# Optimization experiments

Measured on AMD Instinct MI355X. Metric: run time of the kernel, lower is better.

The kernel has to match this reference:

```python
import jax, jax.numpy as jnp
import numpy as np

FEA, DK, H = 768, 64, 12
B, L = 4, 1024
MASK_VAL = -2**15 + 1  # matches torch masked_fill constant


def setup_inputs() -> dict:
    key = jax.random.key(0)
    ks = jax.random.split(key, 16)
    d = {
        'qx': jax.random.normal(ks[0], (B, L, FEA), jnp.float32),
        'kx': jax.random.normal(ks[1], (B, L, FEA), jnp.float32),
        'vx': jax.random.normal(ks[2], (B, L, FEA), jnp.float32),
        'preScores': jax.random.normal(ks[3], (B, H, L, L), jnp.float32),
        'maskPAD': jax.random.randint(ks[4], (B, L, L), 0, 2, jnp.int32),
    }
    s = 1.0 / np.sqrt(FEA)
    d['WQ_w'] = jax.random.normal(ks[5], (H * DK, FEA), jnp.float32) * s
    d['WQ_b'] = jnp.zeros((H * DK,), jnp.float32)
    d['WK_w'] = jax.random.normal(ks[6], (H * DK, FEA), jnp.float32) * s
    d['WK_b'] = jnp.zeros((H * DK,), jnp.float32)
    d['WV_w'] = jax.random.normal(ks[7], (H * DK, FEA), jnp.float32) * s
    d['WV_b'] = jnp.zeros((H * DK,), jnp.float32)
    d['WO_w'] = jax.random.normal(ks[8], (FEA, H * DK), jnp.float32) * s
    d['WO_b'] = jnp.zeros((FEA,), jnp.float32)
    return d


def reference(qx, kx, vx, preScores, maskPAD,
              WQ_w, WQ_b, WK_w, WK_b, WV_w, WV_b, WO_w, WO_b):
    b, l, c = qx.shape
    # projections -> (B, H, L, dk)
    q = (qx @ WQ_w.T + WQ_b).reshape(b, l, H, DK).transpose(0, 2, 1, 3)
    k = (kx @ WK_w.T + WK_b).reshape(b, l, H, DK).transpose(0, 2, 1, 3)
    v = (vx @ WV_w.T + WV_b).reshape(b, l, H, DK).transpose(0, 2, 1, 3)
    scores = jnp.einsum('bhqd,bhkd->bhqk', q, k) / np.sqrt(DK)
    scores = scores + preScores  # RealFormer residual scores
    scores = jnp.where((maskPAD == 0)[:, None, :, :], jnp.float32(MASK_VAL), scores)
    alpha = jax.nn.softmax(scores, axis=3)  # dropout p=0 (eval/deterministic)
    z = jnp.einsum('bhqk,bhkd->bhqd', alpha, v)
    z = z.transpose(0, 2, 1, 3).reshape(b, l, H * DK)
    z = z @ WO_w.T + WO_b
    return z, scores
```

## Files before the change

kernel.cpp:

```cpp
#include <hip/hip_runtime.h>
#include <hip/hip_bf16.h>

#define B_ 4
#define L_ 1024
#define H_ 12
#define DK_ 64
#define FEA_ 768
#define MASKV (-32767.0f)

typedef __attribute__((ext_vector_type(8))) short bf16x8;
typedef __attribute__((ext_vector_type(4))) short s16x4;
typedef __attribute__((ext_vector_type(4))) float f32x4;
typedef unsigned int u32;

__device__ inline short f2bf(float x) {
  __hip_bfloat16 h = __float2bfloat16(x);
  return __builtin_bit_cast(short, h);
}

#define SZX  (4 * 1024 * 768)
#define SZW  (768 * 768)

__global__ __launch_bounds__(256) void k_cvt(
    const float* __restrict__ qx, const float* __restrict__ kx,
    const float* __restrict__ vx,
    const float* __restrict__ Wq, const float* __restrict__ Wk,
    const float* __restrict__ Wv,
    unsigned short* __restrict__ dst)
{
  const size_t SZX4 = SZX / 4, SZW4 = SZW / 4;
  const size_t total4 = 3 * SZX4 + 3 * SZW4;
  for (size_t i4 = (size_t)blockIdx.x * 256 + threadIdx.x; i4 < total4;
       i4 += (size_t)gridDim.x * 256) {
    const float* src; size_t o4; size_t db;
    if (i4 < SZX4)               { src = qx; o4 = i4;               db = 0; }
    else if (i4 < 2 * SZX4)      { src = kx; o4 = i4 - SZX4;        db = (size_t)SZX; }
    else if (i4 < 3 * SZX4)      { src = vx; o4 = i4 - 2 * SZX4;    db = 2 * (size_t)SZX; }
    else if (i4 < 3 * SZX4 + SZW4)     { src = Wq; o4 = i4 - 3 * SZX4;            db = 3 * (size_t)SZX; }
    else if (i4 < 3 * SZX4 + 2 * SZW4) { src = Wk; o4 = i4 - 3 * SZX4 - SZW4;     db = 3 * (size_t)SZX + SZW; }
    else                               { src = Wv; o4 = i4 - 3 * SZX4 - 2 * SZW4; db = 3 * (size_t)SZX + 2 * (size_t)SZW; }
    float4 v = ((const float4*)src)[o4];
    s16x4 r = {f2bf(v.x), f2bf(v.y), f2bf(v.z), f2bf(v.w)};
    *(s16x4*)(dst + db + o4 * 4) = r;
  }
}

__global__ __launch_bounds__(256) void k_cvt2(
    const float* __restrict__ Wo, unsigned short* __restrict__ dst)
{
  size_t i4 = (size_t)blockIdx.x * 256 + threadIdx.x;
  if (i4 < (size_t)SZW / 4) {
    float4 v = ((const float4*)Wo)[i4];
    s16x4 r = {f2bf(v.x), f2bf(v.y), f2bf(v.z), f2bf(v.w)};
    *(s16x4*)(dst + i4 * 4) = r;
  }
}

__global__ __launch_bounds__(256) void k_proj(
    const unsigned short* __restrict__ qxb, const unsigned short* __restrict__ kxb,
    const unsigned short* __restrict__ vxb,
    const unsigned short* __restrict__ Wqb, const unsigned short* __restrict__ Wkb,
    const unsigned short* __restrict__ Wvb,
    const float* __restrict__ bq, const float* __restrict__ bk,
    const float* __restrict__ bv,
    unsigned short* __restrict__ Qb, unsigned short* __restrict__ Kb,
    unsigned short* __restrict__ Vt)
{
  __shared__ short lA[2][64 * 64];
  __shared__ short lB[2][64 * 64];

  const int which = blockIdx.z;
  const unsigned short* __restrict__ Ab = (which == 0) ? qxb : (which == 1) ? kxb : vxb;
  const unsigned short* __restrict__ Wb = (which == 0) ? Wqb : (which == 1) ? Wkb : Wvb;
  const float* __restrict__ bias = (which == 0) ? bq : (which == 1) ? bk : bv;

  const int tid = threadIdx.x;
  const int lane = tid & 63;
  const int wid = tid >> 6;
  const int wr = wid >> 1, wc = wid & 1;
  const int m0 = blockIdx.x * 64;
  const int n0 = blockIdx.y * 64;
  const int g = lane >> 4, qc = lane & 15;
  const int srow = lane >> 3;
  const int spos = lane & 7;

#define PSTAGE(buf, ktof)                                                      \
  {                                                                            \
    _Pragma("unroll")                                                          \
    for (int i_ = 0; i_ < 2; i_++) {                                           \
      int r0_ = wid * 16 + i_ * 8;                                             \
      int row_ = r0_ + srow;                                                   \
      int cs_ = spos ^ (row_ & 7);                                             \
      __builtin_amdgcn_global_load_lds(                                        \
          (const __attribute__((address_space(1))) u32*)(Ab +                  \
              (size_t)(m0 + row_) * FEA_ + (ktof) + cs_ * 8),                  \
          (__attribute__((address_space(3))) u32*)&lA[buf][r0_ * 64],          \
          16, 0, 0);                                                           \
      __builtin_amdgcn_global_load_lds(                                        \
          (const __attribute__((address_space(1))) u32*)(Wb +                  \
              (size_t)(n0 + row_) * FEA_ + (ktof) + cs_ * 8),                  \
          (__attribute__((address_space(3))) u32*)&lB[buf][r0_ * 64],          \
          16, 0, 0);                                                           \
    }                                                                          \
  }

  f32x4 acc[2][2];
#pragma unroll
  for (int i = 0; i < 2; i++)
#pragma unroll
    for (int j = 0; j < 2; j++) acc[i][j] = f32x4{0.f, 0.f, 0.f, 0.f};

  PSTAGE(0, 0);
  asm volatile("s_waitcnt vmcnt(0)" ::: "memory");
  __builtin_amdgcn_s_barrier();

  for (int kt = 0; kt < 12; kt++) {
    const int cur = kt & 1, nxt = cur ^ 1;
    if (kt < 11) PSTAGE(nxt, (kt + 1) * 64);
    __builtin_amdgcn_sched_barrier(0);
    __builtin_amdgcn_s_setprio(1);
#pragma unroll
    for (int s = 0; s < 2; s++) {
      bf16x8 af[2], bfr[2];
#pragma unroll
      for (int i = 0; i < 2; i++) {
        int ar = wr * 32 + i * 16 + qc;
        af[i] = *(const bf16x8*)&lA[cur][ar * 64 + (((s * 4 + g) ^ (ar & 7)) << 3)];
        int br = wc * 32 + i * 16 + qc;
        bfr[i] = *(const bf16x8*)&lB[cur][br * 64 + (((s * 4 + g) ^ (br & 7)) << 3)];
      }
#pragma unroll
      for (int i = 0; i < 2; i++)
#pragma unroll
        for (int j = 0; j < 2; j++)
          acc[i][j] = __builtin_amdgcn_mfma_f32_16x16x32_bf16(af[i], bfr[j], acc[i][j], 0, 0, 0);
    }
    __builtin_amdgcn_s_setprio(0);
    asm volatile("s_waitcnt vmcnt(0)" ::: "memory");
    __builtin_amdgcn_s_barrier();
  }

  const int cn0 = n0 + wc * 32;
  float bv2[2];
#pragma unroll
  for (int j = 0; j < 2; j++) bv2[j] = bias[cn0 + j * 16 + qc];

#pragma unroll
  for (int i = 0; i < 2; i++) {
    int m = m0 + wr * 32 + i * 16 + g * 4;
    int bb = m >> 10;
    int l = m & 1023;
#pragma unroll
    for (int j = 0; j < 2; j++) {
      int n = cn0 + j * 16 + qc;
      int hh = n >> 6, d = n & 63;
      if (which == 2) {
        s16x4 vv = {f2bf(acc[i][j][0] + bv2[j]), f2bf(acc[i][j][1] + bv2[j]),
                    f2bf(acc[i][j][2] + bv2[j]), f2bf(acc[i][j][3] + bv2[j])};
        *(s16x4*)&Vt[(((size_t)bb * H_ + hh) * DK_ + d) * L_ + l] = vv;
      } else {
#pragma unroll
        for (int r = 0; r < 4; r++) {
          unsigned short v = (unsigned short)f2bf(acc[i][j][r] + bv2[j]);
          if (which == 0) {
            Qb[(((size_t)bb * H_ + hh) * L_ + (l + r)) * DK_ + d] = v;
          } else {
            Kb[(((size_t)bb * H_ + hh) * L_ + (l + r)) * DK_ + d] = v;
          }
        }
      }
    }
  }
#undef PSTAGE
}

__global__ __launch_bounds__(256, 3) void k_attn(
    const unsigned short* __restrict__ Qb, const unsigned short* __restrict__ Kb,
    const unsigned short* __restrict__ Vt,
    const float* __restrict__ preScores, const int* __restrict__ maskPAD,
    float* __restrict__ scoresOut, unsigned short* __restrict__ zp)
{
  __shared__ short lK[2][64 * 64];
  __shared__ short lV[2][64 * 64];
  __shared__ short lP[4][16 * 64];

  const int tid = threadIdx.x, lane = tid & 63, wid = tid >> 6;
  const int bi = blockIdx.x;
  const int slot = bi >> 3;
  const int bh_i = (bi & 7) * 6 + (slot >> 4);
  const int qt = slot & 15;
  const int b = bh_i / H_;
  const int h = bh_i % H_;
  const int q0 = qt * 64;
  const int g = lane >> 4, qr = lane & 15;
  const int qrow = q0 + wid * 16 + qr;

  const size_t bh = (size_t)b * H_ + h;
  const unsigned short* __restrict__ Kbh = Kb + bh * L_ * DK_;
  const unsigned short* __restrict__ Vbh = Vt + bh * DK_ * L_;

  const int srow = lane >> 3;
  const int spos = lane & 7;

#define STAGE_KV(buf, kv0)                                                     \
  {                                                                            \
    _Pragma("unroll")                                                          \
    for (int i_ = 0; i_ < 2; i_++) {                                           \
      int r0_ = wid * 16 + i_ * 8;                                             \
      int row_ = r0_ + srow;                                                   \
      int cs_ = spos ^ (row_ & 7);                                             \
      __builtin_amdgcn_global_load_lds(                                        \
          (const __attribute__((address_space(1))) u32*)(Kbh +                 \
              (size_t)((kv0) + row_) * DK_ + cs_ * 8),                         \
          (__attribute__((address_space(3))) u32*)&lK[buf][r0_ * 64],          \
          16, 0, 0);                                                           \
      __builtin_amdgcn_global_load_lds(                                        \
          (const __attribute__((address_space(1))) u32*)(Vbh +                 \
              (size_t)row_ * L_ + (kv0) + cs_ * 8),                            \
          (__attribute__((address_space(3))) u32*)&lV[buf][r0_ * 64],          \
          16, 0, 0);                                                           \
    }                                                                          \
  }

  bf16x8 qf[2];
#pragma unroll
  for (int s = 0; s < 2; s++)
    qf[s] = *(const bf16x8*)(Qb + (bh * L_ + qrow) * DK_ + s * 32 + g * 8);

  f32x4 o[4];
#pragma unroll
  for (int i = 0; i < 4; i++) o[i] = f32x4{0.f, 0.f, 0.f, 0.f};
  float psum = 0.f;

  const size_t psBase = (bh * L_ + qrow) * L_;
  const size_t mkBase = ((size_t)b * L_ + qrow) * L_;

  STAGE_KV(0, 0);
  __builtin_amdgcn_sched_barrier(0);
  float4 psn[4];
  int4 mkn[4];
#pragma unroll
  for (int i = 0; i < 4; i++) {
    psn[i] = *(const float4*)(preScores + psBase + i * 16 + g * 4);
    mkn[i] = *(const int4*)(maskPAD + mkBase + i * 16 + g * 4);
  }
  asm volatile("s_waitcnt vmcnt(8)" ::: "memory");
  __builtin_amdgcn_s_barrier();

  for (int kt = 0; kt < 16; kt++) {
    const int kv0 = kt * 64;
    const int cur = kt & 1, nxt = cur ^ 1;

    if (kt < 15) {
      STAGE_KV(nxt, kv0 + 64);
    }
    __builtin_amdgcn_sched_barrier(0);

    float4 psc[4]; int4 mkc[4];
#pragma unroll
    for (int i = 0; i < 4; i++) { psc[i] = psn[i]; mkc[i] = mkn[i]; }
    if (kt < 15) {
#pragma unroll
      for (int i = 0; i < 4; i++) {
        psn[i] = *(const float4*)(preScores + psBase + kv0 + 64 + i * 16 + g * 4);
        mkn[i] = *(const int4*)(maskPAD + mkBase + kv0 + 64 + i * 16 + g * 4);
      }
    }

    f32x4 st[4];
#pragma unroll
    for (int i = 0; i < 4; i++) st[i] = f32x4{0.f, 0.f, 0.f, 0.f};
    __builtin_amdgcn_s_setprio(1);
#pragma unroll
    for (int s = 0; s < 2; s++) {
#pragma unroll
      for (int i = 0; i < 4; i++) {
        int kr = i * 16 + qr;
        bf16x8 kf = *(const bf16x8*)&lK[cur][kr * 64 + (((s * 4 + g) ^ (kr & 7)) << 3)];
        st[i] = __builtin_amdgcn_mfma_f32_16x16x32_bf16(kf, qf[s], st[i], 0, 0, 0);
      }
    }
    __builtin_amdgcn_s_setprio(0);

#pragma unroll
    for (int i = 0; i < 4; i++) {
      int ko = i * 16 + g * 4;
      float4 sv;
      sv.x = (mkc[i].x == 0) ? MASKV : st[i][0] * 0.125f + psc[i].x;
      sv.y = (mkc[i].y == 0) ? MASKV : st[i][1] * 0.125f + psc[i].y;
      sv.z = (mkc[i].z == 0) ? MASKV : st[i][2] * 0.125f + psc[i].z;
      sv.w = (mkc[i].w == 0) ? MASKV : st[i][3] * 0.125f + psc[i].w;
      *(float4*)(scoresOut + psBase + kv0 + ko) = sv;
      float p0 = __expf(sv.x);
      float p1 = __expf(sv.y);
      float p2 = __expf(sv.z);
      float p3 = __expf(sv.w);
      psum += (p0 + p1) + (p2 + p3);
      s16x4 pw = {f2bf(p0), f2bf(p1), f2bf(p2), f2bf(p3)};
      int c = i * 2 + (g >> 1);
      *(s16x4*)&lP[wid][qr * 64 + ((c ^ (qr & 7)) << 3) + ((g & 1) << 2)] = pw;
    }

    __builtin_amdgcn_s_setprio(1);
#pragma unroll
    for (int s = 0; s < 2; s++) {
      bf16x8 pf = *(const bf16x8*)&lP[wid][qr * 64 + (((s * 4 + g) ^ (qr & 7)) << 3)];
#pragma unroll
      for (int i = 0; i < 4; i++) {
        int vr = i * 16 + qr;
        bf16x8 vf = *(const bf16x8*)&lV[cur][vr * 64 + (((s * 4 + g) ^ (vr & 7)) << 3)];
        o[i] = __builtin_amdgcn_mfma_f32_16x16x32_bf16(vf, pf, o[i], 0, 0, 0);
      }
    }
    __builtin_amdgcn_s_setprio(0);

    asm volatile("s_waitcnt vmcnt(12)" ::: "memory");
    __builtin_amdgcn_s_barrier();
  }

  psum += __shfl_xor(psum, 16);
  psum += __shfl_xor(psum, 32);
  float inv = 1.f / psum;
  size_t zr = ((size_t)b * L_ + qrow) * FEA_ + (size_t)h * DK_;
#pragma unroll
  for (int i = 0; i < 4; i++) {
    s16x4 zw = {f2bf(o[i][0] * inv), f2bf(o[i][1] * inv),
                f2bf(o[i][2] * inv), f2bf(o[i][3] * inv)};
    *(s16x4*)((unsigned short*)zp + zr + i * 16 + g * 4) = zw;
  }
#undef STAGE_KV
}

__global__ __launch_bounds__(256) void k_oproj(
    const unsigned short* __restrict__ zp,
    const unsigned short* __restrict__ Wob, const float* __restrict__ bo,
    float* __restrict__ out)
{
  __shared__ short lA[2][64 * 64];
  __shared__ short lB[2][64 * 64];

  const int tid = threadIdx.x;
  const int lane = tid & 63;
  const int wid = tid >> 6;
  const int wr = wid >> 1, wc = wid & 1;
  const int m0 = blockIdx.x * 64;
  const int n0 = blockIdx.y * 64;
  const int g = lane >> 4, qc = lane & 15;
  const int srow = lane >> 3;
  const int spos = lane & 7;

#define OSTAGE(buf, ktof)                                                      \
  {                                                                            \
    _Pragma("unroll")                                                          \
    for (int i_ = 0; i_ < 2; i_++) {                                           \
      int r0_ = wid * 16 + i_ * 8;                                             \
      int row_ = r0_ + srow;                                                   \
      int cs_ = spos ^ (row_ & 7);                                             \
      __builtin_amdgcn_global_load_lds(                                        \
          (const __attribute__((address_space(1))) u32*)(zp +                  \
              (size_t)(m0 + row_) * FEA_ + (ktof) + cs_ * 8),                  \
          (__attribute__((address_space(3))) u32*)&lA[buf][r0_ * 64],          \
          16, 0, 0);                                                           \
      __builtin_amdgcn_global_load_lds(                                        \
          (const __attribute__((address_space(1))) u32*)(Wob +                 \
              (size_t)(n0 + row_) * FEA_ + (ktof) + cs_ * 8),                  \
          (__attribute__((address_space(3))) u32*)&lB[buf][r0_ * 64],          \
          16, 0, 0);                                                           \
    }                                                                          \
  }

  f32x4 acc[2][2];
#pragma unroll
  for (int i = 0; i < 2; i++)
#pragma unroll
    for (int j = 0; j < 2; j++) acc[i][j] = f32x4{0.f, 0.f, 0.f, 0.f};

  OSTAGE(0, 0);
  asm volatile("s_waitcnt vmcnt(0)" ::: "memory");
  __builtin_amdgcn_s_barrier();

  for (int kt = 0; kt < 12; kt++) {
    const int cur = kt & 1, nxt = cur ^ 1;
    if (kt < 11) OSTAGE(nxt, (kt + 1) * 64);
    __builtin_amdgcn_sched_barrier(0);
    __builtin_amdgcn_s_setprio(1);
#pragma unroll
    for (int s = 0; s < 2; s++) {
      bf16x8 af[2], bfr[2];
#pragma unroll
      for (int i = 0; i < 2; i++) {
        int ar = wr * 32 + i * 16 + qc;
        af[i] = *(const bf16x8*)&lA[cur][ar * 64 + (((s * 4 + g) ^ (ar & 7)) << 3)];
        int br = wc * 32 + i * 16 + qc;
        bfr[i] = *(const bf16x8*)&lB[cur][br * 64 + (((s * 4 + g) ^ (br & 7)) << 3)];
      }
#pragma unroll
      for (int i = 0; i < 2; i++)
#pragma unroll
        for (int j = 0; j < 2; j++)
          acc[i][j] = __builtin_amdgcn_mfma_f32_16x16x32_bf16(af[i], bfr[j], acc[i][j], 0, 0, 0);
    }
    __builtin_amdgcn_s_setprio(0);
    asm volatile("s_waitcnt vmcnt(0)" ::: "memory");
    __builtin_amdgcn_s_barrier();
  }

  const int cn0 = n0 + wc * 32;
  float bv2[2];
#pragma unroll
  for (int j = 0; j < 2; j++) bv2[j] = bo[cn0 + j * 16 + qc];

#pragma unroll
  for (int i = 0; i < 2; i++) {
    int m = m0 + wr * 32 + i * 16 + g * 4;
#pragma unroll
    for (int j = 0; j < 2; j++) {
      int n = cn0 + j * 16 + qc;
#pragma unroll
      for (int r = 0; r < 4; r++) {
        out[(size_t)(m + r) * FEA_ + n] = acc[i][j][r] + bv2[j];
      }
    }
  }
#undef OSTAGE
}

extern "C" void kernel_launch(void* const* d_in, const int* in_sizes, int n_in,
                              void* d_out, int out_size, void* d_ws, size_t ws_size,
                              hipStream_t stream) {
  const float* qx = (const float*)d_in[0];
  const float* kx = (const float*)d_in[1];
  const float* vx = (const float*)d_in[2];
  const float* preScores = (const float*)d_in[3];
  const int* maskPAD = (const int*)d_in[4];
  const float* Wq = (const float*)d_in[5];
  const float* bq = (const float*)d_in[6];
  const float* Wk = (const float*)d_in[7];
  const float* bk = (const float*)d_in[8];
  const float* Wv = (const float*)d_in[9];
  const float* bv = (const float*)d_in[10];
  const float* Wo = (const float*)d_in[11];
  const float* bo = (const float*)d_in[12];

  float* z_out = (float*)d_out;
  float* scores_out = z_out + (size_t)B_ * L_ * FEA_;

  unsigned short* Qb = (unsigned short*)d_ws;
  unsigned short* Kb = Qb + (size_t)B_ * H_ * L_ * DK_;
  unsigned short* Vt = Kb + (size_t)B_ * H_ * L_ * DK_;
  unsigned short* zp = Vt + (size_t)B_ * H_ * L_ * DK_;

  unsigned short* cvtb = (unsigned short*)(scores_out + (50331648 - 5603328));
  const unsigned short* qxb = cvtb;
  const unsigned short* kxb = cvtb + (size_t)SZX;
  const unsigned short* vxb = cvtb + 2 * (size_t)SZX;
  const unsigned short* Wqb = cvtb + 3 * (size_t)SZX;
  const unsigned short* Wkb = cvtb + 3 * (size_t)SZX + (size_t)SZW;
  const unsigned short* Wvb = cvtb + 3 * (size_t)SZX + 2 * (size_t)SZW;

  unsigned short* Wob = Qb;

  k_cvt<<<dim3(1024), 256, 0, stream>>>(qx, kx, vx, Wq, Wk, Wv, cvtb);
  k_proj<<<dim3(64, 12, 3), 256, 0, stream>>>(qxb, kxb, vxb, Wqb, Wkb, Wvb,
                                              bq, bk, bv, Qb, Kb, Vt);
  k_attn<<<dim3(8 * 6 * 16, 1, 1), 256, 0, stream>>>(Qb, Kb, Vt, preScores,
                                                     maskPAD, scores_out, zp);
  k_cvt2<<<dim3(576), 256, 0, stream>>>(Wo, Wob);
  k_oproj<<<dim3(64, 12), 256, 0, stream>>>(zp, Wob, bo, z_out);
}
```

Measured before the change: 169.2 us.

## Transpose scores through LDS to coalesce preScores, mask and scores accesses

The attention kernel used to read preScores and maskPAD and write scores directly in the MFMA accumulator layout, so each lane touched short 16-byte pieces of many different rows. It now stages the QK^T tile in per-wave LDS and reads it back row-major, so 16 lanes cover 64 contiguous floats of one row and the large fp32 streams are fully coalesced. The LDS buffer is shared with the P tile, and the row sums become per-row partials reduced with shuffles and passed through LDS. This adds LDS traffic and shuffles per tile in exchange for better global memory efficiency on the dominant memory streams.

Result: faster. 156.0 us (median of 2 runs) (-7.8%).

```diff
diff --git a/kernel.cpp b/kernel.cpp
--- a/kernel.cpp
+++ b/kernel.cpp
@@ -182,7 +182,7 @@
 {
   __shared__ short lK[2][64 * 64];
   __shared__ short lV[2][64 * 64];
-  __shared__ short lP[4][16 * 64];
+  __shared__ float lU[4][1120];
 
   const int tid = threadIdx.x, lane = tid & 63, wid = tid >> 6;
   const int bi = blockIdx.x;
@@ -194,10 +194,16 @@
   const int q0 = qt * 64;
   const int g = lane >> 4, qr = lane & 15;
   const int qrow = q0 + wid * 16 + qr;
+  const int rhi = lane >> 4, klo = lane & 15;
+  const int rowCg = q0 + wid * 16 + rhi;
 
   const size_t bh = (size_t)b * H_ + h;
   const unsigned short* __restrict__ Kbh = Kb + bh * L_ * DK_;
   const unsigned short* __restrict__ Vbh = Vt + bh * DK_ * L_;
+
+  float* lSw = &lU[wid][0];
+  short* lPw = (short*)&lU[wid][0];
+  float* lLw = &lU[wid][1088];
 
   const int srow = lane >> 3;
   const int spos = lane & 7;
@@ -230,19 +236,19 @@
   f32x4 o[4];
 #pragma unroll
   for (int i = 0; i < 4; i++) o[i] = f32x4{0.f, 0.f, 0.f, 0.f};
-  float psum = 0.f;
-
-  const size_t psBase = (bh * L_ + qrow) * L_;
-  const size_t mkBase = ((size_t)b * L_ + qrow) * L_;
+  float psum[4] = {0.f, 0.f, 0.f, 0.f};
+
+  const size_t psCbase = (bh * L_ + rowCg) * L_ + klo * 4;
+  const size_t mkCbase = ((size_t)b * L_ + rowCg) * L_ + klo * 4;
 
   STAGE_KV(0, 0);
   __builtin_amdgcn_sched_barrier(0);
   float4 psn[4];
   int4 mkn[4];
 #pragma unroll
-  for (int i = 0; i < 4; i++) {
-    psn[i] = *(const float4*)(preScores + psBase + i * 16 + g * 4);
-    mkn[i] = *(const int4*)(maskPAD + mkBase + i * 16 + g * 4);
+  for (int j = 0; j < 4; j++) {
+    psn[j] = *(const float4*)(preScores + psCbase + j * 4096);
+    mkn[j] = *(const int4*)(maskPAD + mkCbase + j * 4096);
   }
   asm volatile("s_waitcnt vmcnt(8)" ::: "memory");
   __builtin_amdgcn_s_barrier();
@@ -258,12 +264,12 @@
 
     float4 psc[4]; int4 mkc[4];
 #pragma unroll
-    for (int i = 0; i < 4; i++) { psc[i] = psn[i]; mkc[i] = mkn[i]; }
+    for (int j = 0; j < 4; j++) { psc[j] = psn[j]; mkc[j] = mkn[j]; }
     if (kt < 15) {
 #pragma unroll
-      for (int i = 0; i < 4; i++) {
-        psn[i] = *(const float4*)(preScores + psBase + kv0 + 64 + i * 16 + g * 4);
-        mkn[i] = *(const int4*)(maskPAD + mkBase + kv0 + 64 + i * 16 + g * 4);
+      for (int j = 0; j < 4; j++) {
+        psn[j] = *(const float4*)(preScores + psCbase + kv0 + 64 + j * 4096);
+        mkn[j] = *(const int4*)(maskPAD + mkCbase + kv0 + 64 + j * 4096);
       }
     }
 
@@ -283,28 +289,36 @@
     __builtin_amdgcn_s_setprio(0);
 
 #pragma unroll
-    for (int i = 0; i < 4; i++) {
-      int ko = i * 16 + g * 4;
+    for (int i = 0; i < 4; i++)
+      *(f32x4*)&lSw[qr * 68 + i * 16 + g * 4] = st[i];
+    f32x4 stc[4];
+#pragma unroll
+    for (int j = 0; j < 4; j++)
+      stc[j] = *(const f32x4*)&lSw[(4 * j + rhi) * 68 + klo * 4];
+
+#pragma unroll
+    for (int j = 0; j < 4; j++) {
       float4 sv;
-      sv.x = (mkc[i].x == 0) ? MASKV : st[i][0] * 0.125f + psc[i].x;
-      sv.y = (mkc[i].y == 0) ? MASKV : st[i][1] * 0.125f + psc[i].y;
-      sv.z = (mkc[i].z == 0) ? MASKV : st[i][2] * 0.125f + psc[i].z;
-      sv.w = (mkc[i].w == 0) ? MASKV : st[i][3] * 0.125f + psc[i].w;
-      *(float4*)(scoresOut + psBase + kv0 + ko) = sv;
+      sv.x = (mkc[j].x == 0) ? MASKV : stc[j][0] * 0.125f + psc[j].x;
+      sv.y = (mkc[j].y == 0) ? MASKV : stc[j][1] * 0.125f + psc[j].y;
+      sv.z = (mkc[j].z == 0) ? MASKV : stc[j][2] * 0.125f + psc[j].z;
+      sv.w = (mkc[j].w == 0) ? MASKV : stc[j][3] * 0.125f + psc[j].w;
+      *(float4*)(scoresOut + psCbase + kv0 + j * 4096) = sv;
       float p0 = __expf(sv.x);
       float p1 = __expf(sv.y);
       float p2 = __expf(sv.z);
       float p3 = __expf(sv.w);
-      psum += (p0 + p1) + (p2 + p3);
+      psum[j] += (p0 + p1) + (p2 + p3);
       s16x4 pw = {f2bf(p0), f2bf(p1), f2bf(p2), f2bf(p3)};
-      int c = i * 2 + (g >> 1);
-      *(s16x4*)&lP[wid][qr * 64 + ((c ^ (qr & 7)) << 3) + ((g & 1) << 2)] = pw;
+      int rL = 4 * j + rhi;
+      int c = klo >> 1, sub = (klo & 1) * 4;
+      *(s16x4*)&lPw[rL * 64 + ((c ^ (rL & 7)) << 3) + sub] = pw;
     }
 
     __builtin_amdgcn_s_setprio(1);
 #pragma unroll
     for (int s = 0; s < 2; s++) {
-      bf16x8 pf = *(const bf16x8*)&lP[wid][qr * 64 + (((s * 4 + g) ^ (qr & 7)) << 3)];
+      bf16x8 pf = *(const bf16x8*)&lPw[qr * 64 + (((s * 4 + g) ^ (qr & 7)) << 3)];
 #pragma unroll
       for (int i = 0; i < 4; i++) {
         int vr = i * 16 + qr;
@@ -318,9 +332,16 @@
     __builtin_amdgcn_s_barrier();
   }
 
-  psum += __shfl_xor(psum, 16);
-  psum += __shfl_xor(psum, 32);
-  float inv = 1.f / psum;
+#pragma unroll
+  for (int j = 0; j < 4; j++) {
+    float v = psum[j];
+    v += __shfl_xor(v, 1);
+    v += __shfl_xor(v, 2);
+    v += __shfl_xor(v, 4);
+    v += __shfl_xor(v, 8);
+    if (klo == 0) lLw[4 * j + rhi] = v;
+  }
+  float inv = 1.f / lLw[qr];
   size_t zr = ((size_t)b * L_ + qrow) * FEA_ + (size_t)h * DK_;
 #pragma unroll
   for (int i = 0; i < 4; i++) {
```
